# Optimization experiments

Measured on AMD Instinct MI355X. Metric: run time of the kernel, lower is better.

## Reference

```python
import jax, jax.numpy as jnp
import numpy as np

EPS = 1e-5  # torch.nn.LayerNorm default


def _layer_norm(h, g, b):
    mu = jnp.mean(h, axis=-1, keepdims=True)
    var = jnp.mean(jnp.square(h - mu), axis=-1, keepdims=True)
    return (h - mu) * jax.lax.rsqrt(var + EPS) * g + b


def setup_inputs() -> dict:
    key = jax.random.key(0)
    ks = jax.random.split(key, 16)
    N, E, D, G, H = 100000, 3200000, 16, 64, 8
    x = jax.random.normal(ks[0], (N, D), dtype=jnp.float32)
    edge_index = jax.random.randint(ks[1], (2, E), 0, N, dtype=jnp.int64)
    vp = jax.random.normal(ks[2], (G, D), dtype=jnp.float32)
    batch = jnp.sort(jax.random.randint(ks[3], (N,), 0, G, dtype=jnp.int64))
    def lin(k, fan_in, fan_out):
        bound = 1.0 / np.sqrt(fan_in)
        kw, kb = jax.random.split(k)
        W = jax.random.uniform(kw, (fan_in, fan_out), jnp.float32, -bound, bound)
        b = jax.random.uniform(kb, (fan_out,), jnp.float32, -bound, bound)
        return W, b
    W1, b1 = lin(ks[4], 3 * D, H)
    W2, b2 = lin(ks[5], H, H)
    W3, b3 = lin(ks[6], H, H)
    W4, b4 = lin(ks[7], H, 1)
    g1 = jnp.ones((H,), jnp.float32); be1 = jnp.zeros((H,), jnp.float32)
    g2 = jnp.ones((H,), jnp.float32); be2 = jnp.zeros((H,), jnp.float32)
    g3 = jnp.ones((H,), jnp.float32); be3 = jnp.zeros((H,), jnp.float32)
    return dict(x=x, edge_index=edge_index, vp=vp, batch=batch,
                W1=W1, b1=b1, g1=g1, be1=be1,
                W2=W2, b2=b2, g2=g2, be2=be2,
                W3=W3, b3=b3, g3=g3, be3=be3,
                W4=W4, b4=b4)


def reference(x, edge_index, vp, batch,
              W1, b1, g1, be1, W2, b2, g2, be2, W3, b3, g3, be3, W4, b4):
    start, end = edge_index[0], edge_index[1]
    # gather node features for both endpoints + per-graph features of the start node's event
    edge_inputs = jnp.concatenate([x[start], x[end], vp[batch[start]]], axis=1)  # [E, 3D]
    h = jnp.tanh(_layer_norm(edge_inputs @ W1 + b1, g1, be1))
    h = jnp.tanh(_layer_norm(h @ W2 + b2, g2, be2))
    h = jnp.tanh(_layer_norm(h @ W3 + b3, g3, be3))
    out = h @ W4 + b4  # [E, 1]
    return out.squeeze(-1)
```

## Files before the change

kernel.cpp:

```cpp
#include <hip/hip_runtime.h>
#include <hip/hip_fp16.h>


struct WPack {
    __half2 w2[32];
    __half2 w3[32];
    __half2 b2p[4], b3p[4];
    __half2 g1p[4], be1p[4];
    __half2 g2p[4], be2p[4];
    __half2 g3p[4], be3p[4];
};

typedef __attribute__((ext_vector_type(8))) _Float16 h8;

__device__ __forceinline__ float fast_tanh(float v) {
    float e = __expf(2.0f * v);
    return fmaf(-2.0f, __builtin_amdgcn_rcpf(e + 1.0f), 1.0f);
}

__global__ __launch_bounds__(256) void node_pre_kernel(
    const float* __restrict__ x,
    const int* __restrict__ batch,
    const float* __restrict__ vp,
    const float* __restrict__ W1,
    const float* __restrict__ b1,
    h8* __restrict__ ya16,
    h8* __restrict__ yb16,
    int N)
{
    int n = blockIdx.x * blockDim.x + threadIdx.x;
    if (n >= N) return;

    const float4* px = reinterpret_cast<const float4*>(x) + (size_t)n * 4;
    float4 x0 = px[0], x1 = px[1], x2 = px[2], x3 = px[3];
    int g = batch[n];
    const float4* pv = reinterpret_cast<const float4*>(vp) + (size_t)g * 4;
    float4 v0 = pv[0], v1 = pv[1], v2 = pv[2], v3 = pv[3];

    float xs[16] = {x0.x, x0.y, x0.z, x0.w, x1.x, x1.y, x1.z, x1.w,
                    x2.x, x2.y, x2.z, x2.w, x3.x, x3.y, x3.z, x3.w};
    float vs[16] = {v0.x, v0.y, v0.z, v0.w, v1.x, v1.y, v1.z, v1.w,
                    v2.x, v2.y, v2.z, v2.w, v3.x, v3.y, v3.z, v3.w};

    float ya[8], yb[8];
#pragma unroll
    for (int j = 0; j < 8; ++j) { ya[j] = b1[j]; yb[j] = 0.0f; }

#pragma unroll
    for (int i = 0; i < 16; ++i) {
        float vx = xs[i];
        float vv = vs[i];
#pragma unroll
        for (int j = 0; j < 8; ++j) {
            ya[j] = fmaf(vx, W1[i * 8 + j], ya[j]);
            ya[j] = fmaf(vv, W1[(32 + i) * 8 + j], ya[j]);
            yb[j] = fmaf(vx, W1[(16 + i) * 8 + j], yb[j]);
        }
    }

    float mua = 0.0f, mub = 0.0f;
#pragma unroll
    for (int j = 0; j < 8; ++j) { mua += ya[j]; mub += yb[j]; }
    mua *= 0.125f; mub *= 0.125f;

    h8 va, vb;
#pragma unroll
    for (int j = 0; j < 8; ++j) {
        va[j] = (_Float16)(ya[j] - mua);
        vb[j] = (_Float16)(yb[j] - mub);
    }
    ya16[n] = va;
    yb16[n] = vb;
}

__global__ void pack_kernel(
    const float* __restrict__ W2, const float* __restrict__ b2,
    const float* __restrict__ W3, const float* __restrict__ b3,
    const float* __restrict__ g1, const float* __restrict__ be1,
    const float* __restrict__ g2, const float* __restrict__ be2,
    const float* __restrict__ g3, const float* __restrict__ be3,
    WPack* __restrict__ wp)
{
    int t = threadIdx.x;
    if (t < 32) {
        wp->w2[t] = __floats2half2_rn(W2[2 * t], W2[2 * t + 1]);
        wp->w3[t] = __floats2half2_rn(W3[2 * t], W3[2 * t + 1]);
    }
    if (t < 4) {
        wp->b2p[t]  = __floats2half2_rn(b2[2 * t],  b2[2 * t + 1]);
        wp->b3p[t]  = __floats2half2_rn(b3[2 * t],  b3[2 * t + 1]);
        wp->g1p[t]  = __floats2half2_rn(g1[2 * t],  g1[2 * t + 1]);
        wp->be1p[t] = __floats2half2_rn(be1[2 * t], be1[2 * t + 1]);
        wp->g2p[t]  = __floats2half2_rn(g2[2 * t],  g2[2 * t + 1]);
        wp->be2p[t] = __floats2half2_rn(be2[2 * t], be2[2 * t + 1]);
        wp->g3p[t]  = __floats2half2_rn(g3[2 * t],  g3[2 * t + 1]);
        wp->be3p[t] = __floats2half2_rn(be3[2 * t], be3[2 * t + 1]);
    }
}

__global__ __launch_bounds__(256) void edge_main_kernel(
    const int* __restrict__ ei,
    const uint4* __restrict__ ya16,
    const uint4* __restrict__ yb16,
    const WPack* __restrict__ wp,
    const float* __restrict__ W4, const float* __restrict__ b4,
    float* __restrict__ out, int E)
{
    int e = blockIdx.x * blockDim.x + threadIdx.x;
    if (e >= E) return;

    int s = ei[e];
    int t = ei[E + e];

    uint4 ua = ya16[s];
    uint4 ub = yb16[t];
    __half2 v[4];
    {
        const __half2* ha = reinterpret_cast<const __half2*>(&ua);
        const __half2* hb2 = reinterpret_cast<const __half2*>(&ub);
#pragma unroll
        for (int k = 0; k < 4; ++k) v[k] = __hadd2(ha[k], hb2[k]);
    }

    __half2 s2 = __hmul2(v[0], v[0]);
    s2 = __hfma2(v[1], v[1], s2);
    s2 = __hfma2(v[2], v[2], s2);
    s2 = __hfma2(v[3], v[3], s2);
    float ss = __low2float(s2) + __high2float(s2);
    float r = __builtin_amdgcn_rsqf(fmaf(ss, 0.125f, 1e-5f));
    __half2 rr2 = __floats2half2_rn(r, r);

    float th[8];
    __half2 hb[8];
#pragma unroll
    for (int k = 0; k < 4; ++k) {
        __half2 rg  = __hmul2(rr2, wp->g1p[k]);
        __half2 arg = __hfma2(v[k], rg, wp->be1p[k]);
        float a0 = fast_tanh(__low2float(arg));
        float a1 = fast_tanh(__high2float(arg));
        th[2 * k] = a0; th[2 * k + 1] = a1;
        hb[2 * k]     = __floats2half2_rn(a0, a0);
        hb[2 * k + 1] = __floats2half2_rn(a1, a1);
    }

    __half2 acc[4];
#pragma unroll
    for (int k = 0; k < 4; ++k) acc[k] = wp->b2p[k];
#pragma unroll
    for (int i = 0; i < 8; ++i) {
#pragma unroll
        for (int k = 0; k < 4; ++k)
            acc[k] = __hfma2(hb[i], wp->w2[i * 4 + k], acc[k]);
    }
    {
        __half2 sm2 = __hadd2(__hadd2(acc[0], acc[1]), __hadd2(acc[2], acc[3]));
        __half2 sq2 = __hmul2(acc[0], acc[0]);
        sq2 = __hfma2(acc[1], acc[1], sq2);
        sq2 = __hfma2(acc[2], acc[2], sq2);
        sq2 = __hfma2(acc[3], acc[3], sq2);
        float sm = __low2float(sm2) + __high2float(sm2);
        float sq = __low2float(sq2) + __high2float(sq2);
        float mu = sm * 0.125f;
        float var = fmaf(sq, 0.125f, -mu * mu);
        float rr = __builtin_amdgcn_rsqf(var + 1e-5f);
        __half2 rrp = __floats2half2_rn(rr, rr);
        float m = -mu * rr;
        __half2 mm2 = __floats2half2_rn(m, m);
#pragma unroll
        for (int k = 0; k < 4; ++k) {
            __half2 rg  = __hmul2(rrp, wp->g2p[k]);
            __half2 c   = __hfma2(mm2, wp->g2p[k], wp->be2p[k]);
            __half2 arg = __hfma2(acc[k], rg, c);
            float a0 = fast_tanh(__low2float(arg));
            float a1 = fast_tanh(__high2float(arg));
            th[2 * k] = a0; th[2 * k + 1] = a1;
            hb[2 * k]     = __floats2half2_rn(a0, a0);
            hb[2 * k + 1] = __floats2half2_rn(a1, a1);
        }
    }

#pragma unroll
    for (int k = 0; k < 4; ++k) acc[k] = wp->b3p[k];
#pragma unroll
    for (int i = 0; i < 8; ++i) {
#pragma unroll
        for (int k = 0; k < 4; ++k)
            acc[k] = __hfma2(hb[i], wp->w3[i * 4 + k], acc[k]);
    }
    {
        __half2 sm2 = __hadd2(__hadd2(acc[0], acc[1]), __hadd2(acc[2], acc[3]));
        __half2 sq2 = __hmul2(acc[0], acc[0]);
        sq2 = __hfma2(acc[1], acc[1], sq2);
        sq2 = __hfma2(acc[2], acc[2], sq2);
        sq2 = __hfma2(acc[3], acc[3], sq2);
        float sm = __low2float(sm2) + __high2float(sm2);
        float sq = __low2float(sq2) + __high2float(sq2);
        float mu = sm * 0.125f;
        float var = fmaf(sq, 0.125f, -mu * mu);
        float rr = __builtin_amdgcn_rsqf(var + 1e-5f);
        __half2 rrp = __floats2half2_rn(rr, rr);
        float m = -mu * rr;
        __half2 mm2 = __floats2half2_rn(m, m);
#pragma unroll
        for (int k = 0; k < 4; ++k) {
            __half2 rg  = __hmul2(rrp, wp->g3p[k]);
            __half2 c   = __hfma2(mm2, wp->g3p[k], wp->be3p[k]);
            __half2 arg = __hfma2(acc[k], rg, c);
            th[2 * k]     = fast_tanh(__low2float(arg));
            th[2 * k + 1] = fast_tanh(__high2float(arg));
        }
    }

    float o = b4[0];
#pragma unroll
    for (int i = 0; i < 8; ++i) o = fmaf(th[i], W4[i], o);

    out[e] = o;
}

__device__ __forceinline__ void ln_tanh8_full(float* h, const float* __restrict__ g,
                                              const float* __restrict__ be) {
    float sm = 0.0f, sq = 0.0f;
#pragma unroll
    for (int j = 0; j < 8; ++j) { sm += h[j]; sq = fmaf(h[j], h[j], sq); }
    float mu = sm * 0.125f;
    float var = fmaf(sq, 0.125f, -mu * mu);
    float rr = __builtin_amdgcn_rsqf(var + 1e-5f);
#pragma unroll
    for (int j = 0; j < 8; ++j)
        h[j] = fast_tanh(fmaf(h[j] - mu, rr * g[j], be[j]));
}

__global__ __launch_bounds__(256) void edge_net_fallback(
    const float* __restrict__ x, const int* __restrict__ ei,
    const float* __restrict__ vp, const int* __restrict__ batch,
    const float* __restrict__ W1, const float* __restrict__ b1,
    const float* __restrict__ g1, const float* __restrict__ be1,
    const float* __restrict__ W2, const float* __restrict__ b2,
    const float* __restrict__ g2, const float* __restrict__ be2,
    const float* __restrict__ W3, const float* __restrict__ b3,
    const float* __restrict__ g3, const float* __restrict__ be3,
    const float* __restrict__ W4, const float* __restrict__ b4,
    float* __restrict__ out, int E)
{
    int e = blockIdx.x * blockDim.x + threadIdx.x;
    if (e >= E) return;
    int s = ei[e], t = ei[E + e];
    int gb = batch[s];
    float in[48];
    const float4* ps = reinterpret_cast<const float4*>(x) + (size_t)s * 4;
    const float4* pt = reinterpret_cast<const float4*>(x) + (size_t)t * 4;
    const float4* pv = reinterpret_cast<const float4*>(vp) + (size_t)gb * 4;
#pragma unroll
    for (int q = 0; q < 4; ++q) {
        float4 a = ps[q];
        in[q*4+0]=a.x; in[q*4+1]=a.y; in[q*4+2]=a.z; in[q*4+3]=a.w;
    }
#pragma unroll
    for (int q = 0; q < 4; ++q) {
        float4 a = pt[q];
        in[16+q*4+0]=a.x; in[16+q*4+1]=a.y; in[16+q*4+2]=a.z; in[16+q*4+3]=a.w;
    }
#pragma unroll
    for (int q = 0; q < 4; ++q) {
        float4 a = pv[q];
        in[32+q*4+0]=a.x; in[32+q*4+1]=a.y; in[32+q*4+2]=a.z; in[32+q*4+3]=a.w;
    }
    float h[8];
#pragma unroll
    for (int j = 0; j < 8; ++j) h[j] = b1[j];
#pragma unroll
    for (int i = 0; i < 48; ++i) {
        float v = in[i];
#pragma unroll
        for (int j = 0; j < 8; ++j) h[j] = fmaf(v, W1[i*8+j], h[j]);
    }
    ln_tanh8_full(h, g1, be1);
    float h2[8];
#pragma unroll
    for (int j = 0; j < 8; ++j) h2[j] = b2[j];
#pragma unroll
    for (int i = 0; i < 8; ++i) {
        float v = h[i];
#pragma unroll
        for (int j = 0; j < 8; ++j) h2[j] = fmaf(v, W2[i*8+j], h2[j]);
    }
    ln_tanh8_full(h2, g2, be2);
    float h3[8];
#pragma unroll
    for (int j = 0; j < 8; ++j) h3[j] = b3[j];
#pragma unroll
    for (int i = 0; i < 8; ++i) {
        float v = h2[i];
#pragma unroll
        for (int j = 0; j < 8; ++j) h3[j] = fmaf(v, W3[i*8+j], h3[j]);
    }
    ln_tanh8_full(h3, g3, be3);
    float o = b4[0];
#pragma unroll
    for (int i = 0; i < 8; ++i) o = fmaf(h3[i], W4[i], o);
    out[e] = o;
}

extern "C" void kernel_launch(void* const* d_in, const int* in_sizes, int n_in,
                              void* d_out, int out_size, void* d_ws, size_t ws_size,
                              hipStream_t stream) {
    const float* x     = (const float*)d_in[0];
    const int*   ei    = (const int*)d_in[1];
    const float* vp    = (const float*)d_in[2];
    const int*   batch = (const int*)d_in[3];
    const float* W1  = (const float*)d_in[4];
    const float* b1  = (const float*)d_in[5];
    const float* g1  = (const float*)d_in[6];
    const float* be1 = (const float*)d_in[7];
    const float* W2  = (const float*)d_in[8];
    const float* b2  = (const float*)d_in[9];
    const float* g2  = (const float*)d_in[10];
    const float* be2 = (const float*)d_in[11];
    const float* W3  = (const float*)d_in[12];
    const float* b3  = (const float*)d_in[13];
    const float* g3  = (const float*)d_in[14];
    const float* be3 = (const float*)d_in[15];
    const float* W4  = (const float*)d_in[16];
    const float* b4  = (const float*)d_in[17];

    int E = in_sizes[1] / 2;
    int N = in_sizes[3];
    float* out = (float*)d_out;

    size_t tab_bytes = (size_t)N * 8 * sizeof(_Float16);
    size_t need = 2 * tab_bytes + sizeof(WPack) + 64;
    if (ws_size >= need) {
        h8* ya16 = (h8*)d_ws;
        h8* yb16 = (h8*)((char*)d_ws + tab_bytes);
        WPack* wp = (WPack*)((char*)d_ws + 2 * tab_bytes);

        int blockA = 256;
        int gridA = (N + blockA - 1) / blockA;
        hipLaunchKernelGGL(node_pre_kernel, dim3(gridA), dim3(blockA), 0, stream,
                           x, batch, vp, W1, b1, ya16, yb16, N);
        hipLaunchKernelGGL(pack_kernel, dim3(1), dim3(64), 0, stream,
                           W2, b2, W3, b3, g1, be1, g2, be2, g3, be3, wp);
        int blockB = 256;
        int gridB = (E + blockB - 1) / blockB;
        hipLaunchKernelGGL(edge_main_kernel, dim3(gridB), dim3(blockB), 0, stream,
                           ei, (const uint4*)ya16, (const uint4*)yb16, wp,
                           W4, b4, out, E);
    } else {
        int block = 256;
        int grid = (E + block - 1) / block;
        hipLaunchKernelGGL(edge_net_fallback, dim3(grid), dim3(block), 0, stream,
                           x, ei, vp, batch,
                           W1, b1, g1, be1, W2, b2, g2, be2, W3, b3, g3, be3,
                           W4, b4, out, E);
    }
}
```

Before: 148.0 us.

## Fold tanh affine transform into weights and process two edges per thread

```diff
diff --git a/kernel.cpp b/kernel.cpp
--- a/kernel.cpp
+++ b/kernel.cpp
@@ -9,9 +9,19 @@
     __half2 g1p[4], be1p[4];
     __half2 g2p[4], be2p[4];
     __half2 g3p[4], be3p[4];
+    float w4[8];
+    float b4a;
 };
 
 typedef __attribute__((ext_vector_type(8))) _Float16 h8;
+
+#if __has_builtin(__builtin_amdgcn_exp2f)
+#define EXP2F(x) __builtin_amdgcn_exp2f(x)
+#else
+#define EXP2F(x) exp2f(x)
+#endif
+
+#define K2LOG2E 2.8853900817779268f
 
 __device__ __forceinline__ float fast_tanh(float v) {
     float e = __expf(2.0f * v);
@@ -79,23 +89,46 @@
     const float* __restrict__ g1, const float* __restrict__ be1,
     const float* __restrict__ g2, const float* __restrict__ be2,
     const float* __restrict__ g3, const float* __restrict__ be3,
+    const float* __restrict__ W4, const float* __restrict__ b4,
     WPack* __restrict__ wp)
 {
-    int t = threadIdx.x;
-    if (t < 32) {
-        wp->w2[t] = __floats2half2_rn(W2[2 * t], W2[2 * t + 1]);
-        wp->w3[t] = __floats2half2_rn(W3[2 * t], W3[2 * t + 1]);
-    }
-    if (t < 4) {
-        wp->b2p[t]  = __floats2half2_rn(b2[2 * t],  b2[2 * t + 1]);
-        wp->b3p[t]  = __floats2half2_rn(b3[2 * t],  b3[2 * t + 1]);
-        wp->g1p[t]  = __floats2half2_rn(g1[2 * t],  g1[2 * t + 1]);
-        wp->be1p[t] = __floats2half2_rn(be1[2 * t], be1[2 * t + 1]);
-        wp->g2p[t]  = __floats2half2_rn(g2[2 * t],  g2[2 * t + 1]);
-        wp->be2p[t] = __floats2half2_rn(be2[2 * t], be2[2 * t + 1]);
-        wp->g3p[t]  = __floats2half2_rn(g3[2 * t],  g3[2 * t + 1]);
-        wp->be3p[t] = __floats2half2_rn(be3[2 * t], be3[2 * t + 1]);
-    }
+    if (threadIdx.x != 0 || blockIdx.x != 0) return;
+#pragma unroll
+    for (int t = 0; t < 32; ++t) {
+        wp->w2[t] = __floats2half2_rn(-2.0f * W2[2 * t], -2.0f * W2[2 * t + 1]);
+        wp->w3[t] = __floats2half2_rn(-2.0f * W3[2 * t], -2.0f * W3[2 * t + 1]);
+    }
+    float cs2[8], cs3[8];
+#pragma unroll
+    for (int j = 0; j < 8; ++j) {
+        float s2 = 0.0f, s3 = 0.0f;
+#pragma unroll
+        for (int i = 0; i < 8; ++i) { s2 += W2[i * 8 + j]; s3 += W3[i * 8 + j]; }
+        cs2[j] = b2[j] + s2;
+        cs3[j] = b3[j] + s3;
+    }
+#pragma unroll
+    for (int t = 0; t < 4; ++t) {
+        wp->b2p[t]  = __floats2half2_rn(cs2[2 * t], cs2[2 * t + 1]);
+        wp->b3p[t]  = __floats2half2_rn(cs3[2 * t], cs3[2 * t + 1]);
+        wp->g1p[t]  = __floats2half2_rn(K2LOG2E * g1[2 * t],  K2LOG2E * g1[2 * t + 1]);
+        wp->be1p[t] = __floats2half2_rn(K2LOG2E * be1[2 * t], K2LOG2E * be1[2 * t + 1]);
+        wp->g2p[t]  = __floats2half2_rn(K2LOG2E * g2[2 * t],  K2LOG2E * g2[2 * t + 1]);
+        wp->be2p[t] = __floats2half2_rn(K2LOG2E * be2[2 * t], K2LOG2E * be2[2 * t + 1]);
+        wp->g3p[t]  = __floats2half2_rn(K2LOG2E * g3[2 * t],  K2LOG2E * g3[2 * t + 1]);
+        wp->be3p[t] = __floats2half2_rn(K2LOG2E * be3[2 * t], K2LOG2E * be3[2 * t + 1]);
+    }
+    float sw4 = 0.0f;
+#pragma unroll
+    for (int i = 0; i < 8; ++i) { wp->w4[i] = -2.0f * W4[i]; sw4 += W4[i]; }
+    wp->b4a = b4[0] + sw4;
+}
+
+__device__ __forceinline__ void site_pair(__half2 arg, float& u0, float& u1) {
+    float a0 = __low2float(arg);
+    float a1 = __high2float(arg);
+    u0 = __builtin_amdgcn_rcpf(EXP2F(a0) + 1.0f);
+    u1 = __builtin_amdgcn_rcpf(EXP2F(a1) + 1.0f);
 }
 
 __global__ __launch_bounds__(256) void edge_main_kernel(
@@ -103,61 +136,85 @@
     const uint4* __restrict__ ya16,
     const uint4* __restrict__ yb16,
     const WPack* __restrict__ wp,
-    const float* __restrict__ W4, const float* __restrict__ b4,
     float* __restrict__ out, int E)
 {
-    int e = blockIdx.x * blockDim.x + threadIdx.x;
-    if (e >= E) return;
-
-    int s = ei[e];
-    int t = ei[E + e];
-
-    uint4 ua = ya16[s];
-    uint4 ub = yb16[t];
-    __half2 v[4];
-    {
-        const __half2* ha = reinterpret_cast<const __half2*>(&ua);
-        const __half2* hb2 = reinterpret_cast<const __half2*>(&ub);
-#pragma unroll
-        for (int k = 0; k < 4; ++k) v[k] = __hadd2(ha[k], hb2[k]);
-    }
-
-    __half2 s2 = __hmul2(v[0], v[0]);
-    s2 = __hfma2(v[1], v[1], s2);
-    s2 = __hfma2(v[2], v[2], s2);
-    s2 = __hfma2(v[3], v[3], s2);
-    float ss = __low2float(s2) + __high2float(s2);
-    float r = __builtin_amdgcn_rsqf(fmaf(ss, 0.125f, 1e-5f));
-    __half2 rr2 = __floats2half2_rn(r, r);
-
-    float th[8];
-    __half2 hb[8];
-#pragma unroll
-    for (int k = 0; k < 4; ++k) {
-        __half2 rg  = __hmul2(rr2, wp->g1p[k]);
-        __half2 arg = __hfma2(v[k], rg, wp->be1p[k]);
-        float a0 = fast_tanh(__low2float(arg));
-        float a1 = fast_tanh(__high2float(arg));
-        th[2 * k] = a0; th[2 * k + 1] = a1;
-        hb[2 * k]     = __floats2half2_rn(a0, a0);
-        hb[2 * k + 1] = __floats2half2_rn(a1, a1);
-    }
-
-    __half2 acc[4];
-#pragma unroll
-    for (int k = 0; k < 4; ++k) acc[k] = wp->b2p[k];
+    int tid = blockIdx.x * blockDim.x + threadIdx.x;
+    int base = tid * 2;
+    if (base >= E) return;
+
+    int s[2], t[2];
+    bool dual = (base + 1 < E);
+    if (dual) {
+        int2 r0 = *reinterpret_cast<const int2*>(ei + base);
+        int2 r1 = *reinterpret_cast<const int2*>(ei + E + base);
+        s[0] = r0.x; s[1] = r0.y;
+        t[0] = r1.x; t[1] = r1.y;
+    } else {
+        s[0] = ei[base]; t[0] = ei[E + base];
+        s[1] = s[0];     t[1] = t[0];
+    }
+
+    uint4 ua[2], ub[2];
+#pragma unroll
+    for (int c = 0; c < 2; ++c) { ua[c] = ya16[s[c]]; ub[c] = yb16[t[c]]; }
+
+    __half2 v[2][4];
+#pragma unroll
+    for (int c = 0; c < 2; ++c) {
+        const __half2* ha = reinterpret_cast<const __half2*>(&ua[c]);
+        const __half2* hb2 = reinterpret_cast<const __half2*>(&ub[c]);
+#pragma unroll
+        for (int k = 0; k < 4; ++k) v[c][k] = __hadd2(ha[k], hb2[k]);
+    }
+
+    __half2 rr2[2];
+#pragma unroll
+    for (int c = 0; c < 2; ++c) {
+        __half2 s2 = __hmul2(v[c][0], v[c][0]);
+        s2 = __hfma2(v[c][1], v[c][1], s2);
+        s2 = __hfma2(v[c][2], v[c][2], s2);
+        s2 = __hfma2(v[c][3], v[c][3], s2);
+        float ss = __low2float(s2) + __high2float(s2);
+        float r = __builtin_amdgcn_rsqf(fmaf(ss, 0.125f, 1e-5f));
+        rr2[c] = __floats2half2_rn(r, r);
+    }
+
+    __half2 hb[2][8];
+#pragma unroll
+    for (int c = 0; c < 2; ++c) {
+#pragma unroll
+        for (int k = 0; k < 4; ++k) {
+            __half2 rg  = __hmul2(rr2[c], wp->g1p[k]);
+            __half2 arg = __hfma2(v[c][k], rg, wp->be1p[k]);
+            float u0, u1;
+            site_pair(arg, u0, u1);
+            hb[c][2 * k]     = __floats2half2_rn(u0, u0);
+            hb[c][2 * k + 1] = __floats2half2_rn(u1, u1);
+        }
+    }
+
+    __half2 acc[2][4];
+#pragma unroll
+    for (int c = 0; c < 2; ++c)
+#pragma unroll
+        for (int k = 0; k < 4; ++k) acc[c][k] = wp->b2p[k];
 #pragma unroll
     for (int i = 0; i < 8; ++i) {
 #pragma unroll
-        for (int k = 0; k < 4; ++k)
-            acc[k] = __hfma2(hb[i], wp->w2[i * 4 + k], acc[k]);
-    }
-    {
-        __half2 sm2 = __hadd2(__hadd2(acc[0], acc[1]), __hadd2(acc[2], acc[3]));
-        __half2 sq2 = __hmul2(acc[0], acc[0]);
-        sq2 = __hfma2(acc[1], acc[1], sq2);
-        sq2 = __hfma2(acc[2], acc[2], sq2);
-        sq2 = __hfma2(acc[3], acc[3], sq2);
+        for (int c = 0; c < 2; ++c)
+#pragma unroll
+            for (int k = 0; k < 4; ++k)
+                acc[c][k] = __hfma2(hb[c][i], wp->w2[i * 4 + k], acc[c][k]);
+    }
+
+#pragma unroll
+    for (int c = 0; c < 2; ++c) {
+        __half2 sm2 = __hadd2(__hadd2(acc[c][0], acc[c][1]),
+                              __hadd2(acc[c][2], acc[c][3]));
+        __half2 sq2 = __hmul2(acc[c][0], acc[c][0]);
+        sq2 = __hfma2(acc[c][1], acc[c][1], sq2);
+        sq2 = __hfma2(acc[c][2], acc[c][2], sq2);
+        sq2 = __hfma2(acc[c][3], acc[c][3], sq2);
         float sm = __low2float(sm2) + __high2float(sm2);
         float sq = __low2float(sq2) + __high2float(sq2);
         float mu = sm * 0.125f;
@@ -169,30 +226,37 @@
 #pragma unroll
         for (int k = 0; k < 4; ++k) {
             __half2 rg  = __hmul2(rrp, wp->g2p[k]);
-            __half2 c   = __hfma2(mm2, wp->g2p[k], wp->be2p[k]);
-            __half2 arg = __hfma2(acc[k], rg, c);
-            float a0 = fast_tanh(__low2float(arg));
-            float a1 = fast_tanh(__high2float(arg));
-            th[2 * k] = a0; th[2 * k + 1] = a1;
-            hb[2 * k]     = __floats2half2_rn(a0, a0);
-            hb[2 * k + 1] = __floats2half2_rn(a1, a1);
+            __half2 cc  = __hfma2(mm2, wp->g2p[k], wp->be2p[k]);
+            __half2 arg = __hfma2(acc[c][k], rg, cc);
+            float u0, u1;
+            site_pair(arg, u0, u1);
+            hb[c][2 * k]     = __floats2half2_rn(u0, u0);
+            hb[c][2 * k + 1] = __floats2half2_rn(u1, u1);
         }
     }
 
 #pragma unroll
-    for (int k = 0; k < 4; ++k) acc[k] = wp->b3p[k];
+    for (int c = 0; c < 2; ++c)
+#pragma unroll
+        for (int k = 0; k < 4; ++k) acc[c][k] = wp->b3p[k];
 #pragma unroll
     for (int i = 0; i < 8; ++i) {
 #pragma unroll
-        for (int k = 0; k < 4; ++k)
-            acc[k] = __hfma2(hb[i], wp->w3[i * 4 + k], acc[k]);
-    }
-    {
-        __half2 sm2 = __hadd2(__hadd2(acc[0], acc[1]), __hadd2(acc[2], acc[3]));
-        __half2 sq2 = __hmul2(acc[0], acc[0]);
-        sq2 = __hfma2(acc[1], acc[1], sq2);
-        sq2 = __hfma2(acc[2], acc[2], sq2);
-        sq2 = __hfma2(acc[3], acc[3], sq2);
+        for (int c = 0; c < 2; ++c)
+#pragma unroll
+            for (int k = 0; k < 4; ++k)
+                acc[c][k] = __hfma2(hb[c][i], wp->w3[i * 4 + k], acc[c][k]);
+    }
+
+    float o[2];
+#pragma unroll
+    for (int c = 0; c < 2; ++c) {
+        __half2 sm2 = __hadd2(__hadd2(acc[c][0], acc[c][1]),
+                              __hadd2(acc[c][2], acc[c][3]));
+        __half2 sq2 = __hmul2(acc[c][0], acc[c][0]);
+        sq2 = __hfma2(acc[c][1], acc[c][1], sq2);
+        sq2 = __hfma2(acc[c][2], acc[c][2], sq2);
+        sq2 = __hfma2(acc[c][3], acc[c][3], sq2);
         float sm = __low2float(sm2) + __high2float(sm2);
         float sq = __low2float(sq2) + __high2float(sq2);
         float mu = sm * 0.125f;
@@ -201,21 +265,25 @@
         __half2 rrp = __floats2half2_rn(rr, rr);
         float m = -mu * rr;
         __half2 mm2 = __floats2half2_rn(m, m);
+        float oo = wp->b4a;
 #pragma unroll
         for (int k = 0; k < 4; ++k) {
             __half2 rg  = __hmul2(rrp, wp->g3p[k]);
-            __half2 c   = __hfma2(mm2, wp->g3p[k], wp->be3p[k]);
-            __half2 arg = __hfma2(acc[k], rg, c);
-            th[2 * k]     = fast_tanh(__low2float(arg));
-            th[2 * k + 1] = fast_tanh(__high2float(arg));
+            __half2 cc  = __hfma2(mm2, wp->g3p[k], wp->be3p[k]);
+            __half2 arg = __hfma2(acc[c][k], rg, cc);
+            float u0, u1;
+            site_pair(arg, u0, u1);
+            oo = fmaf(u0, wp->w4[2 * k], oo);
+            oo = fmaf(u1, wp->w4[2 * k + 1], oo);
         }
-    }
-
-    float o = b4[0];
-#pragma unroll
-    for (int i = 0; i < 8; ++i) o = fmaf(th[i], W4[i], o);
-
-    out[e] = o;
+        o[c] = oo;
+    }
+
+    if (dual) {
+        *reinterpret_cast<float2*>(out + base) = make_float2(o[0], o[1]);
+    } else {
+        out[base] = o[0];
+    }
 }
 
 __device__ __forceinline__ void ln_tanh8_full(float* h, const float* __restrict__ g,
@@ -340,12 +408,12 @@
         hipLaunchKernelGGL(node_pre_kernel, dim3(gridA), dim3(blockA), 0, stream,
                            x, batch, vp, W1, b1, ya16, yb16, N);
         hipLaunchKernelGGL(pack_kernel, dim3(1), dim3(64), 0, stream,
-                           W2, b2, W3, b3, g1, be1, g2, be2, g3, be3, wp);
+                           W2, b2, W3, b3, g1, be1, g2, be2, g3, be3, W4, b4, wp);
+        int pairs = (E + 1) / 2;
         int blockB = 256;
-        int gridB = (E + blockB - 1) / blockB;
+        int gridB = (pairs + blockB - 1) / blockB;
         hipLaunchKernelGGL(edge_main_kernel, dim3(gridB), dim3(blockB), 0, stream,
-                           ei, (const uint4*)ya16, (const uint4*)yb16, wp,
-                           W4, b4, out, E);
+                           ei, (const uint4*)ya16, (const uint4*)yb16, wp, out, E);
     } else {
         int block = 256;
         int grid = (E + block - 1) / block;
```

After: 149.4 us. No clear change (+0.9%).
